# Kernel tuning notes

Measured on AMD Instinct MI355X. Metric: run time of the kernel, lower is better.

The kernel has to match this reference:

```python
import jax, jax.numpy as jnp
import numpy as np

N = 100000      # nodes
E = 1600000     # edges (avg degree 16)
DIN, DH, DOUT = 128, 128, 64


def setup_inputs() -> dict:
    key = jax.random.key(0)
    k0, k1, k2, k3 = jax.random.split(key, 4)
    x = jax.random.normal(k0, (N, DIN), jnp.float32)
    edge_index = jax.random.randint(k1, (2, E), 0, N, dtype=jnp.int64)
    W1 = jax.random.normal(k2, (DIN, DH), jnp.float32) / np.sqrt(DIN).astype(np.float32)
    b1 = jnp.zeros((DH,), jnp.float32)
    W2 = jax.random.normal(k3, (DH, DOUT), jnp.float32) / np.sqrt(DH).astype(np.float32)
    b2 = jnp.zeros((DOUT,), jnp.float32)
    return {"x": x, "edge_index": edge_index, "W1": W1, "b1": b1, "W2": W2, "b2": b2}


def reference(x, edge_index, W1, b1, W2, b2):
    n = x.shape[0]
    # PyG GCNConv: add self-loops, symmetric normalization deg^-1/2 A_hat deg^-1/2
    loops = jnp.arange(n, dtype=edge_index.dtype)
    src = jnp.concatenate([edge_index[0], loops])  # message sources
    dst = jnp.concatenate([edge_index[1], loops])  # aggregation targets
    deg = jax.ops.segment_sum(jnp.ones(src.shape, x.dtype), dst, num_segments=n)
    dinv = jnp.where(deg > 0, jax.lax.rsqrt(deg), 0.0)
    norm = dinv[src] * dinv[dst]                    # [E+N]

    def gcn_conv(h, W, b):
        h = h @ W                                   # dense transform first (PyG order)
        msg = h[src] * norm[:, None]                # gather + scale
        return jax.ops.segment_sum(msg, dst, num_segments=n) + b

    h = jax.nn.relu(gcn_conv(x, W1, b1))
    # F.dropout is identity in eval mode (self.training == False)
    return gcn_conv(h, W2, b2)
```

## Files before the change

### kernel.cpp

```cpp
#include <hip/hip_runtime.h>

#define DIN 128
#define DH  128
#define DOUT 64


__device__ inline unsigned bf16rne(float f) {
    unsigned u = __float_as_uint(f);
    return (u + 0x7fffu + ((u >> 16) & 1u)) >> 16;
}

__device__ inline void acc8(float* a, uint4 v) {
    a[0] += __uint_as_float(v.x << 16); a[1] += __uint_as_float(v.x & 0xffff0000u);
    a[2] += __uint_as_float(v.y << 16); a[3] += __uint_as_float(v.y & 0xffff0000u);
    a[4] += __uint_as_float(v.z << 16); a[5] += __uint_as_float(v.z & 0xffff0000u);
    a[6] += __uint_as_float(v.w << 16); a[7] += __uint_as_float(v.w & 0xffff0000u);
}


__global__ void k_count_rank(const int* __restrict__ dst, int* __restrict__ cnt,
                             int* __restrict__ rank, int E, int pad) {
    int e = blockIdx.x * 256 + threadIdx.x;
    if (e < E) rank[e] = atomicAdd(&cnt[dst[e] * pad], 1);
}

__global__ void k_dinv(const int* __restrict__ cnt, float* __restrict__ dinv, int n, int pad) {
    int i = blockIdx.x * 256 + threadIdx.x;
    if (i < n) dinv[i] = rsqrtf((float)(cnt[i * pad] + 1));
}

__global__ void k_scan_partial(const int* __restrict__ cnt, int* __restrict__ excl,
                               int* __restrict__ bsum, int n, int pad) {
    __shared__ int sd[256];
    int t = threadIdx.x;
    int base = blockIdx.x * 1024 + t * 4;
    int v0 = (base + 0 < n) ? cnt[(base + 0) * pad] : 0;
    int v1 = (base + 1 < n) ? cnt[(base + 1) * pad] : 0;
    int v2 = (base + 2 < n) ? cnt[(base + 2) * pad] : 0;
    int v3 = (base + 3 < n) ? cnt[(base + 3) * pad] : 0;
    int s = v0 + v1 + v2 + v3;
    sd[t] = s;
    __syncthreads();
    for (int off = 1; off < 256; off <<= 1) {
        int x = (t >= off) ? sd[t - off] : 0;
        __syncthreads();
        sd[t] += x;
        __syncthreads();
    }
    int incl = sd[t];
    if (t == 255) bsum[blockIdx.x] = incl;
    int run = incl - s;
    if (base + 0 < n) excl[base + 0] = run;  run += v0;
    if (base + 1 < n) excl[base + 1] = run;  run += v1;
    if (base + 2 < n) excl[base + 2] = run;  run += v2;
    if (base + 3 < n) excl[base + 3] = run;
}

__global__ void k_scan_bsum(int* __restrict__ bsum, int nb) {
    __shared__ int sd[256];
    int t = threadIdx.x;
    int v = (t < nb) ? bsum[t] : 0;
    sd[t] = v;
    __syncthreads();
    for (int off = 1; off < 256; off <<= 1) {
        int x = (t >= off) ? sd[t - off] : 0;
        __syncthreads();
        sd[t] += x;
        __syncthreads();
    }
    if (t < nb) bsum[t] = sd[t] - v;
}

__global__ void k_finalize(int* __restrict__ rowstart, const int* __restrict__ bsum,
                           int n, int E) {
    int i = blockIdx.x * 256 + threadIdx.x;
    if (i < n) rowstart[i] += bsum[i >> 10];
    if (i == 0) rowstart[n] = E;
}

__global__ void k_fill2(const int* __restrict__ src, const int* __restrict__ dst,
                        const int* __restrict__ rank, const int* __restrict__ rowstart,
                        int* __restrict__ adj, int E) {
    int e = blockIdx.x * 256 + threadIdx.x;
    if (e < E) adj[rowstart[dst[e]] + rank[e]] = src[e];
}


__global__ void k_gemm_scaled(const float* __restrict__ A, const float* __restrict__ W,
                              const float* __restrict__ dinv, unsigned short* __restrict__ S,
                              int M, int ncols) {
    __shared__ float xs[32 * 132];
    __shared__ float ws[128 * 64];
    int tid = threadIdx.x;
    int row0 = blockIdx.x * 32;
    int j0   = blockIdx.y * 64;

    #pragma unroll
    for (int i = 0; i < 4; i++) {
        int idx = tid + 256 * i;
        int r = idx >> 5;
        int kq = idx & 31;
        float4 val = make_float4(0.f, 0.f, 0.f, 0.f);
        int row = row0 + r;
        if (row < M) val = *(const float4*)(A + (size_t)row * 128 + kq * 4);
        *(float4*)(xs + r * 132 + kq * 4) = val;
    }
    #pragma unroll
    for (int i = 0; i < 8; i++) {
        int idx = tid + 256 * i;
        int k = idx >> 4;
        int jq = idx & 15;
        float4 val = *(const float4*)(W + (size_t)k * ncols + j0 + jq * 4);
        *(float4*)(ws + k * 64 + jq * 4) = val;
    }
    __syncthreads();

    int tx = tid & 15;
    int ty = tid >> 4;
    float acc[2][4] = {};
    #pragma unroll 8
    for (int k = 0; k < 128; k++) {
        float4 b = *(const float4*)(ws + k * 64 + tx * 4);
        float a0 = xs[(ty * 2 + 0) * 132 + k];
        float a1 = xs[(ty * 2 + 1) * 132 + k];
        acc[0][0] += a0 * b.x; acc[0][1] += a0 * b.y; acc[0][2] += a0 * b.z; acc[0][3] += a0 * b.w;
        acc[1][0] += a1 * b.x; acc[1][1] += a1 * b.y; acc[1][2] += a1 * b.z; acc[1][3] += a1 * b.w;
    }

    #pragma unroll
    for (int r = 0; r < 2; r++) {
        int row = row0 + ty * 2 + r;
        if (row < M) {
            float dv = dinv[row];
            uint2 o;
            o.x = bf16rne(dv * acc[r][0]) | (bf16rne(dv * acc[r][1]) << 16);
            o.y = bf16rne(dv * acc[r][2]) | (bf16rne(dv * acc[r][3]) << 16);
            *(uint2*)(S + (size_t)row * ncols + j0 + tx * 4) = o;
        }
    }
}


template <bool RELU>
__global__ void k_agg128(const unsigned short* __restrict__ S, const int* __restrict__ rowstart,
                         const int* __restrict__ adj, const float* __restrict__ dinv,
                         const float* __restrict__ bias, float* __restrict__ out, int n) {
    int wave = threadIdx.x >> 6;
    int lane = threadIdx.x & 63;
    int node = blockIdx.x * 4 + wave;
    if (node >= n) return;
    int start = rowstart[node];
    int end   = rowstart[node + 1];
    int g  = lane >> 4;
    int fo = lane & 15;

    const uint4* S4 = (const uint4*)S;
    float a0[8] = {}, a1[8] = {};

    while (start < end) {
        int cnt = end - start;
        if (cnt > 64) cnt = 64;
        int nb = adj[start + (lane < cnt ? lane : cnt - 1)];
        int t = 0;
        for (; t + 16 <= cnt; t += 16) {
            int jA = __shfl(nb, t + 0  + g);
            int jB = __shfl(nb, t + 4  + g);
            int jC = __shfl(nb, t + 8  + g);
            int jD = __shfl(nb, t + 12 + g);
            uint4 mA = S4[(size_t)jA * 16 + fo];
            uint4 mB = S4[(size_t)jB * 16 + fo];
            uint4 mC = S4[(size_t)jC * 16 + fo];
            uint4 mD = S4[(size_t)jD * 16 + fo];
            acc8(a0, mA); acc8(a1, mB); acc8(a0, mC); acc8(a1, mD);
        }
        for (; t + 4 <= cnt; t += 4) {
            int j = __shfl(nb, t + g);
            uint4 m = S4[(size_t)j * 16 + fo];
            acc8(a0, m);
        }
        if (t < cnt) {
            int i1 = t + g;
            int j = __shfl(nb, i1 < cnt ? i1 : cnt - 1);
            uint4 m = S4[(size_t)j * 16 + fo];
            if (i1 < cnt) acc8(a1, m);
        }
        start += 64;
    }

    float acc[8];
    #pragma unroll
    for (int i = 0; i < 8; i++) {
        float v = a0[i] + a1[i];
        v += __shfl_xor(v, 16);
        v += __shfl_xor(v, 32);
        acc[i] = v;
    }

    uint4 selfu = ((const uint4*)S)[(size_t)node * 16 + fo];
    float self[8] = {};
    acc8(self, selfu);
    float dv = dinv[node];
    float4 bb0 = ((const float4*)bias)[fo * 2 + 0];
    float4 bb1 = ((const float4*)bias)[fo * 2 + 1];
    float o[8];
    o[0] = dv * (acc[0] + self[0]) + bb0.x;
    o[1] = dv * (acc[1] + self[1]) + bb0.y;
    o[2] = dv * (acc[2] + self[2]) + bb0.z;
    o[3] = dv * (acc[3] + self[3]) + bb0.w;
    o[4] = dv * (acc[4] + self[4]) + bb1.x;
    o[5] = dv * (acc[5] + self[5]) + bb1.y;
    o[6] = dv * (acc[6] + self[6]) + bb1.z;
    o[7] = dv * (acc[7] + self[7]) + bb1.w;
    if (RELU) {
        #pragma unroll
        for (int i = 0; i < 8; i++) o[i] = fmaxf(o[i], 0.f);
    }
    if (g == 0) {
        float4* op = (float4*)(out + (size_t)node * 128 + fo * 8);
        op[0] = make_float4(o[0], o[1], o[2], o[3]);
        op[1] = make_float4(o[4], o[5], o[6], o[7]);
    }
}

__global__ void k_agg64(const unsigned short* __restrict__ S, const int* __restrict__ rowstart,
                        const int* __restrict__ adj, const float* __restrict__ dinv,
                        const float* __restrict__ bias, float* __restrict__ out, int n) {
    int wave = threadIdx.x >> 6;
    int lane = threadIdx.x & 63;
    int node = blockIdx.x * 4 + wave;
    if (node >= n) return;
    int start = rowstart[node];
    int end   = rowstart[node + 1];
    int g  = lane >> 3;
    int fo = lane & 7;

    const uint4* S4 = (const uint4*)S;
    float a0[8] = {}, a1[8] = {};

    while (start < end) {
        int cnt = end - start;
        if (cnt > 64) cnt = 64;
        int nb = adj[start + (lane < cnt ? lane : cnt - 1)];
        int t = 0;
        for (; t + 32 <= cnt; t += 32) {
            int jA = __shfl(nb, t + 0  + g);
            int jB = __shfl(nb, t + 8  + g);
            int jC = __shfl(nb, t + 16 + g);
            int jD = __shfl(nb, t + 24 + g);
            uint4 mA = S4[(size_t)jA * 8 + fo];
            uint4 mB = S4[(size_t)jB * 8 + fo];
            uint4 mC = S4[(size_t)jC * 8 + fo];
            uint4 mD = S4[(size_t)jD * 8 + fo];
            acc8(a0, mA); acc8(a1, mB); acc8(a0, mC); acc8(a1, mD);
        }
        for (; t + 8 <= cnt; t += 8) {
            int j = __shfl(nb, t + g);
            uint4 m = S4[(size_t)j * 8 + fo];
            acc8(a0, m);
        }
        if (t < cnt) {
            int i1 = t + g;
            int j = __shfl(nb, i1 < cnt ? i1 : cnt - 1);
            uint4 m = S4[(size_t)j * 8 + fo];
            if (i1 < cnt) acc8(a1, m);
        }
        start += 64;
    }

    float acc[8];
    #pragma unroll
    for (int i = 0; i < 8; i++) {
        float v = a0[i] + a1[i];
        v += __shfl_xor(v, 8);
        v += __shfl_xor(v, 16);
        v += __shfl_xor(v, 32);
        acc[i] = v;
    }

    uint4 selfu = ((const uint4*)S)[(size_t)node * 8 + fo];
    float self[8] = {};
    acc8(self, selfu);
    float dv = dinv[node];
    float4 bb0 = ((const float4*)bias)[fo * 2 + 0];
    float4 bb1 = ((const float4*)bias)[fo * 2 + 1];
    float o[8];
    o[0] = dv * (acc[0] + self[0]) + bb0.x;
    o[1] = dv * (acc[1] + self[1]) + bb0.y;
    o[2] = dv * (acc[2] + self[2]) + bb0.z;
    o[3] = dv * (acc[3] + self[3]) + bb0.w;
    o[4] = dv * (acc[4] + self[4]) + bb1.x;
    o[5] = dv * (acc[5] + self[5]) + bb1.y;
    o[6] = dv * (acc[6] + self[6]) + bb1.z;
    o[7] = dv * (acc[7] + self[7]) + bb1.w;
    if (g == 0) {
        float4* op = (float4*)(out + (size_t)node * 64 + fo * 8);
        op[0] = make_float4(o[0], o[1], o[2], o[3]);
        op[1] = make_float4(o[4], o[5], o[6], o[7]);
    }
}


extern "C" void kernel_launch(void* const* d_in, const int* in_sizes, int n_in,
                              void* d_out, int out_size, void* d_ws, size_t ws_size,
                              hipStream_t stream) {
    const float* x  = (const float*)d_in[0];
    const int*   ei = (const int*)d_in[1];
    const float* W1 = (const float*)d_in[2];
    const float* b1 = (const float*)d_in[3];
    const float* W2 = (const float*)d_in[4];
    const float* b2 = (const float*)d_in[5];
    float* out = (float*)d_out;

    int N = in_sizes[0] / DIN;
    int E = in_sizes[1] / 2;
    const int* esrc = ei;
    const int* edst = ei + E;

    size_t fixed = (size_t)N * 128 * 2
                 + (size_t)N * 128 * 4
                 + (size_t)N * 4
                 + (size_t)(N + 1) * 4
                 + (size_t)E * 4 * 2
                 + 1024 * 4 + 8 * 256;
    int PAD = (fixed + (size_t)N * 16 * 4 <= ws_size) ? 16 : 1;

    char* wsb = (char*)d_ws;
    size_t off = 0;
    auto alloc = [&](size_t bytes) {
        void* p = wsb + off;
        off = (off + bytes + 255) & ~(size_t)255;
        return p;
    };
    unsigned short* S = (unsigned short*)alloc((size_t)N * 128 * 2);
    float* H1       = (float*)alloc((size_t)N * 128 * 4);
    float* dinv     = (float*)alloc((size_t)N * 4);
    int*   rowstart = (int*)alloc((size_t)(N + 1) * 4);
    int*   adj      = (int*)alloc((size_t)E * 4);
    int*   rank     = (int*)alloc((size_t)E * 4);
    int*   cnt      = (int*)alloc((size_t)N * PAD * 4);
    int*   bsum     = (int*)alloc(1024 * 4);

    int eb = (E + 255) / 256;
    int nb = (N + 255) / 256;
    int sb = (N + 1023) / 1024;

    hipMemsetAsync(cnt, 0, (size_t)N * PAD * 4, stream);
    k_count_rank<<<eb, 256, 0, stream>>>(edst, cnt, rank, E, PAD);
    k_dinv<<<nb, 256, 0, stream>>>(cnt, dinv, N, PAD);
    k_scan_partial<<<sb, 256, 0, stream>>>(cnt, rowstart, bsum, N, PAD);
    k_scan_bsum<<<1, 256, 0, stream>>>(bsum, sb);
    k_finalize<<<nb, 256, 0, stream>>>(rowstart, bsum, N, E);
    k_fill2<<<eb, 256, 0, stream>>>(esrc, edst, rank, rowstart, adj, E);

    dim3 g1((N + 31) / 32, DH / 64);
    k_gemm_scaled<<<g1, 256, 0, stream>>>(x, W1, dinv, S, N, DH);
    int ab = (N + 3) / 4;
    k_agg128<true><<<ab, 256, 0, stream>>>(S, rowstart, adj, dinv, b1, H1, N);

    dim3 g2((N + 31) / 32, DOUT / 64);
    k_gemm_scaled<<<g2, 256, 0, stream>>>(H1, W2, dinv, S, N, DOUT);
    k_agg64<<<ab, 256, 0, stream>>>(S, rowstart, adj, dinv, b2, out, N);
}
```

Before: 309.4 us.

## Replace FP32 SIMT GEMMs with split-bf16 MFMA GEMMs

Replaces the shared-memory FP32 FMA GEMM with a matrix-core kernel that splits inputs and weights into bf16 hi/lo parts and issues three MFMA 16x16x32 bf16 ops per tile, keeping accuracy close to FP32. Weights are pre-split and transposed by a small new kernel on each call. The aim is to cut GEMM compute time. The cost is extra per-element conversion work, 2-byte scattered stores of the output, and B fragments loaded straight from global memory.

```diff
diff --git a/kernel.cpp b/kernel.cpp
--- a/kernel.cpp
+++ b/kernel.cpp
@@ -3,6 +3,9 @@
 #define DIN 128
 #define DH  128
 #define DOUT 64
+
+typedef __attribute__((ext_vector_type(8))) short bf16x8;
+typedef __attribute__((ext_vector_type(4))) float f32x4;
 
 
 __device__ inline unsigned bf16rne(float f) {
@@ -86,56 +89,74 @@
 }
 
 
-__global__ void k_gemm_scaled(const float* __restrict__ A, const float* __restrict__ W,
-                              const float* __restrict__ dinv, unsigned short* __restrict__ S,
-                              int M, int ncols) {
-    __shared__ float xs[32 * 132];
-    __shared__ float ws[128 * 64];
-    int tid = threadIdx.x;
-    int row0 = blockIdx.x * 32;
-    int j0   = blockIdx.y * 64;
-
-    #pragma unroll
-    for (int i = 0; i < 4; i++) {
-        int idx = tid + 256 * i;
-        int r = idx >> 5;
-        int kq = idx & 31;
-        float4 val = make_float4(0.f, 0.f, 0.f, 0.f);
-        int row = row0 + r;
-        if (row < M) val = *(const float4*)(A + (size_t)row * 128 + kq * 4);
-        *(float4*)(xs + r * 132 + kq * 4) = val;
-    }
-    #pragma unroll
-    for (int i = 0; i < 8; i++) {
-        int idx = tid + 256 * i;
-        int k = idx >> 4;
-        int jq = idx & 15;
-        float4 val = *(const float4*)(W + (size_t)k * ncols + j0 + jq * 4);
-        *(float4*)(ws + k * 64 + jq * 4) = val;
-    }
-    __syncthreads();
-
-    int tx = tid & 15;
-    int ty = tid >> 4;
-    float acc[2][4] = {};
-    #pragma unroll 8
-    for (int k = 0; k < 128; k++) {
-        float4 b = *(const float4*)(ws + k * 64 + tx * 4);
-        float a0 = xs[(ty * 2 + 0) * 132 + k];
-        float a1 = xs[(ty * 2 + 1) * 132 + k];
-        acc[0][0] += a0 * b.x; acc[0][1] += a0 * b.y; acc[0][2] += a0 * b.z; acc[0][3] += a0 * b.w;
-        acc[1][0] += a1 * b.x; acc[1][1] += a1 * b.y; acc[1][2] += a1 * b.z; acc[1][3] += a1 * b.w;
-    }
-
-    #pragma unroll
-    for (int r = 0; r < 2; r++) {
-        int row = row0 + ty * 2 + r;
+__global__ void k_wsplit(const float* __restrict__ W, unsigned short* __restrict__ Wt_hi,
+                         unsigned short* __restrict__ Wt_lo, int N) {
+    int idx = blockIdx.x * 256 + threadIdx.x;
+    if (idx >= N * 128) return;
+    int n = idx >> 7;
+    int k = idx & 127;
+    float v = W[(size_t)k * N + n];
+    unsigned h = bf16rne(v);
+    float hf = __uint_as_float(h << 16);
+    unsigned l = bf16rne(v - hf);
+    Wt_hi[idx] = (unsigned short)h;
+    Wt_lo[idx] = (unsigned short)l;
+}
+
+
+template <int NCOLS>
+__global__ void k_gemm_mfma(const float* __restrict__ A,
+                            const unsigned short* __restrict__ Wt_hi,
+                            const unsigned short* __restrict__ Wt_lo,
+                            const float* __restrict__ dinv,
+                            unsigned short* __restrict__ S, int M) {
+    constexpr int NT = NCOLS / 16;
+    int wave = threadIdx.x >> 6;
+    int lane = threadIdx.x & 63;
+    int row0 = blockIdx.x * 64 + wave * 16;
+    int arow = row0 + (lane & 15);
+    if (arow >= M) arow = M - 1;
+    int kfrag = (lane >> 4) * 8;
+    int bcol = lane & 15;
+
+    f32x4 acc[NT];
+    #pragma unroll
+    for (int t = 0; t < NT; t++) acc[t] = (f32x4){0.f, 0.f, 0.f, 0.f};
+
+    #pragma unroll
+    for (int ks = 0; ks < 4; ks++) {
+        const float* ap = A + (size_t)arow * 128 + ks * 32 + kfrag;
+        float4 av0 = *(const float4*)ap;
+        float4 av1 = *(const float4*)(ap + 4);
+        float av[8] = {av0.x, av0.y, av0.z, av0.w, av1.x, av1.y, av1.z, av1.w};
+        bf16x8 ahi, alo;
+        #pragma unroll
+        for (int j = 0; j < 8; j++) {
+            unsigned h = bf16rne(av[j]);
+            float hf = __uint_as_float(h << 16);
+            ahi[j] = (short)h;
+            alo[j] = (short)bf16rne(av[j] - hf);
+        }
+        #pragma unroll
+        for (int t = 0; t < NT; t++) {
+            size_t boff = (size_t)(t * 16 + bcol) * 128 + ks * 32 + kfrag;
+            bf16x8 bhi = *(const bf16x8*)(Wt_hi + boff);
+            bf16x8 blo = *(const bf16x8*)(Wt_lo + boff);
+            acc[t] = __builtin_amdgcn_mfma_f32_16x16x32_bf16(ahi, bhi, acc[t], 0, 0, 0);
+            acc[t] = __builtin_amdgcn_mfma_f32_16x16x32_bf16(ahi, blo, acc[t], 0, 0, 0);
+            acc[t] = __builtin_amdgcn_mfma_f32_16x16x32_bf16(alo, bhi, acc[t], 0, 0, 0);
+        }
+    }
+
+    int srow0 = row0 + (lane >> 4) * 4;
+    #pragma unroll
+    for (int r = 0; r < 4; r++) {
+        int row = srow0 + r;
         if (row < M) {
             float dv = dinv[row];
-            uint2 o;
-            o.x = bf16rne(dv * acc[r][0]) | (bf16rne(dv * acc[r][1]) << 16);
-            o.y = bf16rne(dv * acc[r][2]) | (bf16rne(dv * acc[r][3]) << 16);
-            *(uint2*)(S + (size_t)row * ncols + j0 + tx * 4) = o;
+            #pragma unroll
+            for (int t = 0; t < NT; t++)
+                S[(size_t)row * NCOLS + t * 16 + bcol] = (unsigned short)bf16rne(dv * acc[t][r]);
         }
     }
 }
@@ -321,7 +342,8 @@
                  + (size_t)N * 4
                  + (size_t)(N + 1) * 4
                  + (size_t)E * 4 * 2
-                 + 1024 * 4 + 8 * 256;
+                 + (128 + 64) * 128 * 2 * 2
+                 + 1024 * 4 + 16 * 256;
     int PAD = (fixed + (size_t)N * 16 * 4 <= ws_size) ? 16 : 1;
 
     char* wsb = (char*)d_ws;
@@ -337,12 +359,19 @@
     int*   rowstart = (int*)alloc((size_t)(N + 1) * 4);
     int*   adj      = (int*)alloc((size_t)E * 4);
     int*   rank     = (int*)alloc((size_t)E * 4);
+    unsigned short* wt1h = (unsigned short*)alloc(128 * 128 * 2);
+    unsigned short* wt1l = (unsigned short*)alloc(128 * 128 * 2);
+    unsigned short* wt2h = (unsigned short*)alloc(64 * 128 * 2);
+    unsigned short* wt2l = (unsigned short*)alloc(64 * 128 * 2);
     int*   cnt      = (int*)alloc((size_t)N * PAD * 4);
     int*   bsum     = (int*)alloc(1024 * 4);
 
     int eb = (E + 255) / 256;
     int nb = (N + 255) / 256;
     int sb = (N + 1023) / 1024;
+
+    k_wsplit<<<(128 * 128) / 256, 256, 0, stream>>>(W1, wt1h, wt1l, 128);
+    k_wsplit<<<(64 * 128) / 256, 256, 0, stream>>>(W2, wt2h, wt2l, 64);
 
     hipMemsetAsync(cnt, 0, (size_t)N * PAD * 4, stream);
     k_count_rank<<<eb, 256, 0, stream>>>(edst, cnt, rank, E, PAD);
@@ -352,12 +381,12 @@
     k_finalize<<<nb, 256, 0, stream>>>(rowstart, bsum, N, E);
     k_fill2<<<eb, 256, 0, stream>>>(esrc, edst, rank, rowstart, adj, E);
 
-    dim3 g1((N + 31) / 32, DH / 64);
-    k_gemm_scaled<<<g1, 256, 0, stream>>>(x, W1, dinv, S, N, DH);
+    int gb = (N + 63) / 64;
     int ab = (N + 3) / 4;
+
+    k_gemm_mfma<128><<<gb, 256, 0, stream>>>(x, wt1h, wt1l, dinv, S, N);
     k_agg128<true><<<ab, 256, 0, stream>>>(S, rowstart, adj, dinv, b1, H1, N);
 
-    dim3 g2((N + 31) / 32, DOUT / 64);
-    k_gemm_scaled<<<g2, 256, 0, stream>>>(H1, W2, dinv, S, N, DOUT);
+    k_gemm_mfma<64><<<gb, 256, 0, stream>>>(H1, wt2h, wt2l, dinv, S, N);
     k_agg64<<<ab, 256, 0, stream>>>(S, rowstart, adj, dinv, b2, out, N);
 }
```

After: 312.8 us. Within noise of the previous version (+1.1%).
